# Kernel optimization log

Hardware: AMD Instinct MI355X
Metric: run time of the kernel (lower is better)

The kernel has to match this reference:

```python
import jax, jax.numpy as jnp
import numpy as np

B = 2048
V = 50257
T = 64
D = 32
N_IN = 128
N_OUT = 128
N_HID = 1500
N_LAYERS = 5
N_BIAS = 2
K = 45  # int(edge_prob * n_nodes) fixed in-degree per receiving node
HID_PER_LAYER = N_HID // N_LAYERS  # 300
N_RECV = N_HID + N_OUT  # 1628 receiving nodes (hidden + output)


def _build_graph(rng):
    """Topological random wiring: each receiving node picks K predecessors
    among all earlier nodes (inputs, bias, earlier hidden layers)."""
    src_rows = []
    avail = N_IN + N_BIAS  # nodes available before first hidden layer
    for _ in range(N_LAYERS):
        src_rows.append(rng.integers(0, avail, size=(HID_PER_LAYER, K)))
        avail += HID_PER_LAYER
    src_rows.append(rng.integers(0, avail, size=(N_OUT, K)))  # output nodes
    return np.concatenate(src_rows, axis=0).astype(np.int32)  # [N_RECV, K]


def setup_inputs() -> dict:
    key = jax.random.key(0)
    ks = jax.random.split(key, 6)
    rng = np.random.default_rng(0)
    ids = jax.random.randint(ks[0], (B, T), 0, V, dtype=jnp.int32)
    token_emb = jax.random.normal(ks[1], (V, D), dtype=jnp.float32) * 0.02
    in_w = jax.random.normal(ks[2], (N_IN, T * D), dtype=jnp.float32) / np.sqrt(T * D)
    in_b = jnp.zeros((N_IN,), dtype=jnp.float32)
    src_idx = jnp.asarray(_build_graph(rng))  # [N_RECV, K] int32
    rwnn_w = jax.random.normal(ks[3], (N_RECV, K), dtype=jnp.float32) / np.sqrt(K)
    out_w = jax.random.normal(ks[4], (V, N_OUT), dtype=jnp.float32) / np.sqrt(N_OUT)
    out_b = jnp.zeros((V,), dtype=jnp.float32)
    return {"ids": ids, "token_emb": token_emb, "in_w": in_w, "in_b": in_b,
            "src_idx": src_idx, "rwnn_w": rwnn_w, "out_w": out_w, "out_b": out_b}


def _rwnn_forward(x, src_idx, rwnn_w):
    """x: [B, N_IN] -> [B, N_OUT]. Sparse random-wired DAG forward."""
    b = x.shape[0]
    vals = jnp.concatenate([x, jnp.ones((b, N_BIAS), dtype=x.dtype)], axis=1)
    off = 0
    for _ in range(N_LAYERS):
        s = src_idx[off:off + HID_PER_LAYER]          # [300, K]
        w = rwnn_w[off:off + HID_PER_LAYER]           # [300, K]
        gathered = vals[:, s]                          # [B, 300, K] irregular gather
        new = jnp.tanh(jnp.einsum('bnk,nk->bn', gathered, w))
        vals = jnp.concatenate([vals, new], axis=1)
        off += HID_PER_LAYER
    s = src_idx[off:off + N_OUT]
    w = rwnn_w[off:off + N_OUT]
    return jnp.tanh(jnp.einsum('bnk,nk->bn', vals[:, s], w))  # [B, N_OUT]


def reference(ids, token_emb, in_w, in_b, src_idx, rwnn_w, out_w, out_b):
    emb = token_emb[ids]                     # [B, T, D]
    flat = emb.reshape(emb.shape[0], T * D)  # [B, T*D]
    x = flat @ in_w.T + in_b                 # [B, N_IN]
    h = _rwnn_forward(x, src_idx, rwnn_w)    # [B, N_OUT]
    logits = h @ out_w.T + out_b             # [B, V]
    return logits
```

## Files before the change

kernel.cpp:

```cpp
#include <hip/hip_runtime.h>

#define B_SZ   2048
#define V_SZ   50257
#define TD     2048
#define NIN    128
#define NOUT   128
#define NRECV  1628
#define KDEG   45
#define KPAD   48
#define HPL    300
#define VALSN  1632

typedef __bf16 bf16x8 __attribute__((ext_vector_type(8)));
typedef float  floatx16 __attribute__((ext_vector_type(16)));

__device__ __forceinline__ unsigned short f2bf(float f) {
  unsigned u = __float_as_uint(f);
  u += 0x7fffu + ((u >> 16) & 1u);
  return (unsigned short)(u >> 16);
}

#define P0 1048576
#define P1 1608224
#define P2 65536
#define P3 65536
#define P4 78144
#define PREP_TOTAL (P0 + P1 + P2 + P3 + P4)
#define PREP_BLOCKS ((PREP_TOTAL + 255) / 256)

__global__ __launch_bounds__(256) void prep_kernel(
    const int* __restrict__ ids, const float* __restrict__ temb,
    const float* __restrict__ in_w, const float* __restrict__ in_b,
    const int* __restrict__ src, const float* __restrict__ rw,
    const float* __restrict__ out_w,
    unsigned short* __restrict__ flatb, unsigned short* __restrict__ inwb,
    unsigned short* __restrict__ outwb, float* __restrict__ x,
    int* __restrict__ iw) {
  int i = blockIdx.x * 256 + threadIdx.x;
  if (i < P0) {
    int bt = i >> 3, d4 = i & 7;
    int id = ids[bt];
    float4 v = *(const float4*)(temb + id * 32 + d4 * 4);
    ushort4 o; o.x = f2bf(v.x); o.y = f2bf(v.y); o.z = f2bf(v.z); o.w = f2bf(v.w);
    *(ushort4*)(flatb + (size_t)i * 4) = o;
    return;
  }
  i -= P0;
  if (i < P1) {
    float4 v = ((const float4*)out_w)[i];
    ushort4 o; o.x = f2bf(v.x); o.y = f2bf(v.y); o.z = f2bf(v.z); o.w = f2bf(v.w);
    *(ushort4*)(outwb + (size_t)i * 4) = o;
    return;
  }
  i -= P1;
  if (i < P2) {
    float4 v = ((const float4*)in_w)[i];
    ushort4 o; o.x = f2bf(v.x); o.y = f2bf(v.y); o.z = f2bf(v.z); o.w = f2bf(v.w);
    *(ushort4*)(inwb + (size_t)i * 4) = o;
    return;
  }
  i -= P2;
  if (i < P3) {
    float4 bv = ((const float4*)in_b)[i & 31];
    ((float4*)x)[i] = bv;
    return;
  }
  i -= P3;
  if (i < P4) {
    int r = i / KPAD, k = i - r * KPAD;
    int idx = 0; unsigned wb = 0;
    if (k < KDEG) {
      idx = src[r * KDEG + k];
      wb = __float_as_uint(rw[r * KDEG + k]);
    }
    iw[(size_t)i * 2] = idx;
    iw[(size_t)i * 2 + 1] = (int)wb;
  }
}

__global__ __launch_bounds__(256) void gemm1_kernel(
    const __bf16* __restrict__ flatb, const __bf16* __restrict__ inwb,
    float* __restrict__ x) {
  int tid = threadIdx.x;
  int wv = tid >> 6, lane = tid & 63;
  int row = lane & 31, half = lane >> 5;
  int m0 = blockIdx.x * 32;
  int n0 = wv * 32;
  int k0 = blockIdx.y * 512;
  const __bf16* ap = flatb + (size_t)(m0 + row) * TD + k0 + half * 8;
  const __bf16* bp = inwb + (size_t)(n0 + row) * TD + k0 + half * 8;
  floatx16 acc = (floatx16)0.0f;
#pragma unroll 8
  for (int s = 0; s < 32; ++s) {
    bf16x8 a = *(const bf16x8*)(ap + s * 16);
    bf16x8 b = *(const bf16x8*)(bp + s * 16);
    acc = __builtin_amdgcn_mfma_f32_32x32x16_bf16(a, b, acc, 0, 0, 0);
  }
  int col = n0 + row;
#pragma unroll
  for (int r = 0; r < 16; ++r) {
    int mrow = (r & 3) + 8 * (r >> 2) + 4 * half;
    atomicAdd(&x[(m0 + mrow) * NIN + col], acc[r]);
  }
}

__global__ __launch_bounds__(256) void rwnn_kernel(
    const float* __restrict__ x, const int* __restrict__ iw,
    unsigned short* __restrict__ hb) {
  __shared__ float vals[VALSN * 8];
  int tid = threadIdx.x;
  int b0 = blockIdx.x * 8;
  {
    int p = tid & 7, n = tid >> 3;
    for (int nn = n; nn < NIN; nn += 32)
      vals[nn * 8 + p] = x[(b0 + p) * NIN + nn];
    if (tid < 16) vals[(NIN + (tid >> 3)) * 8 + (tid & 7)] = 1.0f;
  }
  __syncthreads();
  int g = tid >> 1;
  int pb = (tid & 1) * 4;
  int base = NIN + 2;
  int off = 0;
  for (int layer = 0; layer < 5; ++layer) {
    for (int r = g; r < HPL; r += 128) {
      const int4* q4 = (const int4*)(iw) + (size_t)(off + r) * (KPAD / 2);
      float s0 = 0.f, s1 = 0.f, s2 = 0.f, s3 = 0.f;
#pragma unroll
      for (int k4 = 0; k4 < KPAD / 2; ++k4) {
        int4 q = q4[k4];
        float4 v0 = *(const float4*)(&vals[q.x * 8 + pb]);
        float w0 = __int_as_float(q.y);
        s0 += v0.x * w0; s1 += v0.y * w0; s2 += v0.z * w0; s3 += v0.w * w0;
        float4 v1 = *(const float4*)(&vals[q.z * 8 + pb]);
        float w1 = __int_as_float(q.w);
        s0 += v1.x * w1; s1 += v1.y * w1; s2 += v1.z * w1; s3 += v1.w * w1;
      }
      float4 o;
      o.x = tanhf(s0); o.y = tanhf(s1); o.z = tanhf(s2); o.w = tanhf(s3);
      *(float4*)(&vals[(base + r) * 8 + pb]) = o;
    }
    __syncthreads();
    off += HPL; base += HPL;
  }
  {
    int r = g;
    const int4* q4 = (const int4*)(iw) + (size_t)(off + r) * (KPAD / 2);
    float s0 = 0.f, s1 = 0.f, s2 = 0.f, s3 = 0.f;
#pragma unroll
    for (int k4 = 0; k4 < KPAD / 2; ++k4) {
      int4 q = q4[k4];
      float4 v0 = *(const float4*)(&vals[q.x * 8 + pb]);
      float w0 = __int_as_float(q.y);
      s0 += v0.x * w0; s1 += v0.y * w0; s2 += v0.z * w0; s3 += v0.w * w0;
      float4 v1 = *(const float4*)(&vals[q.z * 8 + pb]);
      float w1 = __int_as_float(q.w);
      s0 += v1.x * w1; s1 += v1.y * w1; s2 += v1.z * w1; s3 += v1.w * w1;
    }
    hb[(b0 + pb + 0) * NOUT + r] = f2bf(tanhf(s0));
    hb[(b0 + pb + 1) * NOUT + r] = f2bf(tanhf(s1));
    hb[(b0 + pb + 2) * NOUT + r] = f2bf(tanhf(s2));
    hb[(b0 + pb + 3) * NOUT + r] = f2bf(tanhf(s3));
  }
}

__global__ __launch_bounds__(256) void gemm3_kernel(
    const __bf16* __restrict__ h, const __bf16* __restrict__ wv,
    const float* __restrict__ out_b, float* __restrict__ out) {
  int tid = threadIdx.x;
  int wvid = tid >> 6, lane = tid & 63;
  int row = lane & 31, half = lane >> 5;
  int m0 = blockIdx.x * 32;
  int v0 = blockIdx.y * 128 + wvid * 32;
  int vr = v0 + row;
  int vc = vr < V_SZ ? vr : V_SZ - 1;
  const __bf16* ap = h + (size_t)(m0 + row) * NOUT + half * 8;
  const __bf16* bp = wv + (size_t)vc * NOUT + half * 8;
  floatx16 acc = (floatx16)0.0f;
#pragma unroll
  for (int s = 0; s < 8; ++s) {
    bf16x8 a = *(const bf16x8*)(ap + s * 16);
    bf16x8 b = *(const bf16x8*)(bp + s * 16);
    acc = __builtin_amdgcn_mfma_f32_32x32x16_bf16(a, b, acc, 0, 0, 0);
  }
  if (vr < V_SZ) {
    float bias = out_b[vr];
#pragma unroll
    for (int r = 0; r < 16; ++r) {
      int mrow = (r & 3) + 8 * (r >> 2) + 4 * half;
      out[(size_t)(m0 + mrow) * V_SZ + vr] = acc[r] + bias;
    }
  }
}

extern "C" void kernel_launch(void* const* d_in, const int* in_sizes, int n_in,
                              void* d_out, int out_size, void* d_ws, size_t ws_size,
                              hipStream_t stream) {
  const int*   ids   = (const int*)d_in[0];
  const float* temb  = (const float*)d_in[1];
  const float* in_w  = (const float*)d_in[2];
  const float* in_b  = (const float*)d_in[3];
  const int*   src   = (const int*)d_in[4];
  const float* rw    = (const float*)d_in[5];
  const float* out_w = (const float*)d_in[6];
  const float* out_b = (const float*)d_in[7];
  float* out = (float*)d_out;

  char* ws = (char*)d_ws;
  unsigned short* flatb = (unsigned short*)(ws);
  unsigned short* inwb  = (unsigned short*)(ws + 8388608);
  unsigned short* outwb = (unsigned short*)(ws + 8912896);
  float*          x     = (float*)(ws + 21778688);
  unsigned short* hb    = (unsigned short*)(ws + 22827264);
  int*            iw    = (int*)(ws + 23351552);

  prep_kernel<<<PREP_BLOCKS, 256, 0, stream>>>(ids, temb, in_w, in_b, src, rw,
                                               out_w, flatb, inwb, outwb, x, iw);
  gemm1_kernel<<<dim3(64, 4), 256, 0, stream>>>((const __bf16*)flatb,
                                                (const __bf16*)inwb, x);
  rwnn_kernel<<<256, 256, 0, stream>>>(x, iw, hb);
  gemm3_kernel<<<dim3(64, 393), 256, 0, stream>>>((const __bf16*)hb,
                                                  (const __bf16*)outwb, out_b, out);
}
```

Measured before the change: 648.9 us.

## Reduce gemm1 split-K in shared memory, widen RWNN blocks, use fast tanh

gemm1 now splits K across the four waves of a block and reduces the partials in shared memory, adding the bias directly. This removes the global atomics and the bias-initialisation pass in the prep kernel. The RWNN kernel moves to 512 threads, each handling 2 batch columns instead of 4, which doubles the thread-level parallelism in the serial DAG layers. tanhf is replaced by an exp2/rcp approximation, which changes precision slightly.

```diff
diff --git a/kernel.cpp b/kernel.cpp
--- a/kernel.cpp
+++ b/kernel.cpp
@@ -20,21 +20,25 @@
   return (unsigned short)(u >> 16);
 }
 
+__device__ __forceinline__ float tanh_fast(float v) {
+  float e = __builtin_amdgcn_exp2f(v * 2.88539008177793f);
+  return 1.0f - 2.0f * __builtin_amdgcn_rcpf(1.0f + e);
+}
+
 #define P0 1048576
 #define P1 1608224
 #define P2 65536
-#define P3 65536
 #define P4 78144
-#define PREP_TOTAL (P0 + P1 + P2 + P3 + P4)
+#define PREP_TOTAL (P0 + P1 + P2 + P4)
 #define PREP_BLOCKS ((PREP_TOTAL + 255) / 256)
 
 __global__ __launch_bounds__(256) void prep_kernel(
     const int* __restrict__ ids, const float* __restrict__ temb,
-    const float* __restrict__ in_w, const float* __restrict__ in_b,
+    const float* __restrict__ in_w,
     const int* __restrict__ src, const float* __restrict__ rw,
     const float* __restrict__ out_w,
     unsigned short* __restrict__ flatb, unsigned short* __restrict__ inwb,
-    unsigned short* __restrict__ outwb, float* __restrict__ x,
+    unsigned short* __restrict__ outwb,
     int* __restrict__ iw) {
   int i = blockIdx.x * 256 + threadIdx.x;
   if (i < P0) {
@@ -60,12 +64,6 @@
     return;
   }
   i -= P2;
-  if (i < P3) {
-    float4 bv = ((const float4*)in_b)[i & 31];
-    ((float4*)x)[i] = bv;
-    return;
-  }
-  i -= P3;
   if (i < P4) {
     int r = i / KPAD, k = i - r * KPAD;
     int idx = 0; unsigned wb = 0;
@@ -80,13 +78,14 @@
 
 __global__ __launch_bounds__(256) void gemm1_kernel(
     const __bf16* __restrict__ flatb, const __bf16* __restrict__ inwb,
-    float* __restrict__ x) {
+    const float* __restrict__ in_b, float* __restrict__ x) {
+  __shared__ float red[4 * 32 * 32];
   int tid = threadIdx.x;
   int wv = tid >> 6, lane = tid & 63;
   int row = lane & 31, half = lane >> 5;
   int m0 = blockIdx.x * 32;
-  int n0 = wv * 32;
-  int k0 = blockIdx.y * 512;
+  int n0 = blockIdx.y * 32;
+  int k0 = wv * 512;
   const __bf16* ap = flatb + (size_t)(m0 + row) * TD + k0 + half * 8;
   const __bf16* bp = inwb + (size_t)(n0 + row) * TD + k0 + half * 8;
   floatx16 acc = (floatx16)0.0f;
@@ -96,15 +95,23 @@
     bf16x8 b = *(const bf16x8*)(bp + s * 16);
     acc = __builtin_amdgcn_mfma_f32_32x32x16_bf16(a, b, acc, 0, 0, 0);
   }
-  int col = n0 + row;
 #pragma unroll
   for (int r = 0; r < 16; ++r) {
     int mrow = (r & 3) + 8 * (r >> 2) + 4 * half;
-    atomicAdd(&x[(m0 + mrow) * NIN + col], acc[r]);
-  }
-}
-
-__global__ __launch_bounds__(256) void rwnn_kernel(
+    red[wv * 1024 + mrow * 32 + row] = acc[r];
+  }
+  __syncthreads();
+#pragma unroll
+  for (int p = 0; p < 4; ++p) {
+    int idx = p * 256 + tid;
+    int ml = idx >> 5, nl = idx & 31;
+    float s = red[idx] + red[1024 + idx] + red[2048 + idx] + red[3072 + idx]
+            + in_b[n0 + nl];
+    x[(size_t)(m0 + ml) * NIN + n0 + nl] = s;
+  }
+}
+
+__global__ __launch_bounds__(512) void rwnn_kernel(
     const float* __restrict__ x, const int* __restrict__ iw,
     unsigned short* __restrict__ hb) {
   __shared__ float vals[VALSN * 8];
@@ -112,32 +119,31 @@
   int b0 = blockIdx.x * 8;
   {
     int p = tid & 7, n = tid >> 3;
-    for (int nn = n; nn < NIN; nn += 32)
-      vals[nn * 8 + p] = x[(b0 + p) * NIN + nn];
+    vals[n * 8 + p] = x[(b0 + p) * NIN + n];
+    vals[(n + 64) * 8 + p] = x[(b0 + p) * NIN + n + 64];
     if (tid < 16) vals[(NIN + (tid >> 3)) * 8 + (tid & 7)] = 1.0f;
   }
   __syncthreads();
-  int g = tid >> 1;
-  int pb = (tid & 1) * 4;
+  int g = tid >> 2;
+  int pq = (tid & 3) * 2;
   int base = NIN + 2;
   int off = 0;
   for (int layer = 0; layer < 5; ++layer) {
     for (int r = g; r < HPL; r += 128) {
       const int4* q4 = (const int4*)(iw) + (size_t)(off + r) * (KPAD / 2);
-      float s0 = 0.f, s1 = 0.f, s2 = 0.f, s3 = 0.f;
+      float s0 = 0.f, s1 = 0.f;
 #pragma unroll
       for (int k4 = 0; k4 < KPAD / 2; ++k4) {
         int4 q = q4[k4];
-        float4 v0 = *(const float4*)(&vals[q.x * 8 + pb]);
+        float2 v0 = *(const float2*)(&vals[q.x * 8 + pq]);
         float w0 = __int_as_float(q.y);
-        s0 += v0.x * w0; s1 += v0.y * w0; s2 += v0.z * w0; s3 += v0.w * w0;
-        float4 v1 = *(const float4*)(&vals[q.z * 8 + pb]);
+        s0 += v0.x * w0; s1 += v0.y * w0;
+        float2 v1 = *(const float2*)(&vals[q.z * 8 + pq]);
         float w1 = __int_as_float(q.w);
-        s0 += v1.x * w1; s1 += v1.y * w1; s2 += v1.z * w1; s3 += v1.w * w1;
+        s0 += v1.x * w1; s1 += v1.y * w1;
       }
-      float4 o;
-      o.x = tanhf(s0); o.y = tanhf(s1); o.z = tanhf(s2); o.w = tanhf(s3);
-      *(float4*)(&vals[(base + r) * 8 + pb]) = o;
+      float2 o; o.x = tanh_fast(s0); o.y = tanh_fast(s1);
+      *(float2*)(&vals[(base + r) * 8 + pq]) = o;
     }
     __syncthreads();
     off += HPL; base += HPL;
@@ -145,21 +151,19 @@
   {
     int r = g;
     const int4* q4 = (const int4*)(iw) + (size_t)(off + r) * (KPAD / 2);
-    float s0 = 0.f, s1 = 0.f, s2 = 0.f, s3 = 0.f;
+    float s0 = 0.f, s1 = 0.f;
 #pragma unroll
     for (int k4 = 0; k4 < KPAD / 2; ++k4) {
       int4 q = q4[k4];
-      float4 v0 = *(const float4*)(&vals[q.x * 8 + pb]);
+      float2 v0 = *(const float2*)(&vals[q.x * 8 + pq]);
       float w0 = __int_as_float(q.y);
-      s0 += v0.x * w0; s1 += v0.y * w0; s2 += v0.z * w0; s3 += v0.w * w0;
-      float4 v1 = *(const float4*)(&vals[q.z * 8 + pb]);
+      s0 += v0.x * w0; s1 += v0.y * w0;
+      float2 v1 = *(const float2*)(&vals[q.z * 8 + pq]);
       float w1 = __int_as_float(q.w);
-      s0 += v1.x * w1; s1 += v1.y * w1; s2 += v1.z * w1; s3 += v1.w * w1;
-    }
-    hb[(b0 + pb + 0) * NOUT + r] = f2bf(tanhf(s0));
-    hb[(b0 + pb + 1) * NOUT + r] = f2bf(tanhf(s1));
-    hb[(b0 + pb + 2) * NOUT + r] = f2bf(tanhf(s2));
-    hb[(b0 + pb + 3) * NOUT + r] = f2bf(tanhf(s3));
+      s0 += v1.x * w1; s1 += v1.y * w1;
+    }
+    hb[(b0 + pq + 0) * NOUT + r] = f2bf(tanh_fast(s0));
+    hb[(b0 + pq + 1) * NOUT + r] = f2bf(tanh_fast(s1));
   }
 }
 
@@ -213,11 +217,11 @@
   unsigned short* hb    = (unsigned short*)(ws + 22827264);
   int*            iw    = (int*)(ws + 23351552);
 
-  prep_kernel<<<PREP_BLOCKS, 256, 0, stream>>>(ids, temb, in_w, in_b, src, rw,
-                                               out_w, flatb, inwb, outwb, x, iw);
+  prep_kernel<<<PREP_BLOCKS, 256, 0, stream>>>(ids, temb, in_w, src, rw,
+                                               out_w, flatb, inwb, outwb, iw);
   gemm1_kernel<<<dim3(64, 4), 256, 0, stream>>>((const __bf16*)flatb,
-                                                (const __bf16*)inwb, x);
-  rwnn_kernel<<<256, 256, 0, stream>>>(x, iw, hb);
+                                                (const __bf16*)inwb, in_b, x);
+  rwnn_kernel<<<256, 512, 0, stream>>>(x, iw, hb);
   gemm3_kernel<<<dim3(64, 393), 256, 0, stream>>>((const __bf16*)hb,
                                                   (const __bf16*)outwb, out_b, out);
 }
```

After: 633.5 us. 1.02x faster.
